# Kernel optimization log

Hardware: AMD Instinct MI355X
Metric: run time of the kernel (lower is better)

The kernel has to match this reference:

```python
import jax, jax.numpy as jnp
import numpy as np

DELTA_VAR = 0.5
DELTA_DIST = 1.5
ALPHA, BETA, GAMMA = 1.0, 1.0, 0.001
NUM_CLUSTERS = 16  # labels in [0, 16); all assumed present per sample (N >> C)

B, F, N = 32, 8, 131072


def _l1(x, axis):
    return jnp.sum(jnp.abs(x), axis=axis)  # norm=1 in the original module


def _discriminative_loss(x, target):
    # x: (B, F, N) float, target: (B, N) int labels in [0, C)
    b, f, n = x.shape
    c = NUM_CLUSTERS
    # flatten batch+cluster into one segment id space
    seg = (target + jnp.arange(b, dtype=target.dtype)[:, None] * c).reshape(-1)  # (B*N,)
    x_flat = x.transpose(0, 2, 1).reshape(b * n, f)  # (B*N, F)

    sums = jax.ops.segment_sum(x_flat, seg, num_segments=b * c)              # (B*C, F)
    counts = jax.ops.segment_sum(jnp.ones((b * n,), x.dtype), seg, num_segments=b * c)
    present = counts > 0
    safe_cnt = jnp.where(present, counts, 1.0)
    means_c = sums / safe_cnt[:, None]                                        # (B*C, F) per-cluster means

    # per-point cluster mean (== c_means tensor in torch, shape (B,F,N) there)
    means_pt = means_c[seg]                                                   # (B*N, F)

    # variance term: hinge(||x - mean||_1 - delta_var)^2, averaged per cluster, summed
    var = jnp.maximum(_l1(x_flat - means_pt, axis=1) - DELTA_VAR, 0.0) ** 2   # (B*N,)
    var_sums = jax.ops.segment_sum(var, seg, num_segments=b * c)
    # NOTE: torch version's division by num_clusters is a discarded no-op -> only /bs
    var_term = jnp.sum(jnp.where(present, var_sums / safe_cnt, 0.0)) / b

    # distance term: torch indexes c_means[i][:, unique_labels]; with labels 0..C-1
    # present, unique == arange(C), i.e. the per-point means at point indices 0..C-1
    mc = means_pt.reshape(b, n, f)[:, :c, :]                                  # (B, C, F)
    d = _l1(mc[:, :, None, :] - mc[:, None, :, :], axis=-1)                   # (B, C, C)
    margin = 2.0 * DELTA_DIST * (1.0 - jnp.eye(c, dtype=x.dtype))             # (C, C)
    dist = jnp.sum(jnp.maximum(margin[None] - d, 0.0) ** 2, axis=(1, 2)) / (c * (c - 1))
    dist_term = jnp.sum(dist) / b

    # regularization: mean over (distinct) cluster means of their L1 norm
    mcC = means_c.reshape(b, c, f)
    reg_term = jnp.sum(jnp.mean(_l1(mcC, axis=-1), axis=1)) / b

    return ALPHA * var_term + BETA * dist_term + GAMMA * reg_term


def setup_inputs() -> dict:
    key = jax.random.key(0)
    kx, kt = jax.random.split(key)
    x = jax.random.normal(kx, (B, F, N), dtype=jnp.float32)
    target = jax.random.randint(kt, (B, N), 0, NUM_CLUSTERS, dtype=jnp.int64)
    return {"input": x, "target": target}


def reference(input, target):
    return _discriminative_loss(input, target)
```

## Files before the change

kernel.cpp:

```cpp
#include <hip/hip_runtime.h>

#define BB 32
#define FF 8
#define NN 131072
#define CC 16

#define CHUNKS 64
#define POINTS (NN / CHUNKS)
#define NBLK   (CHUNKS * BB)

constexpr float DELTA_VAR  = 0.5f;
constexpr float DELTA_DIST = 1.5f;
constexpr float ALPHA = 1.0f, BETA = 1.0f, GAMMA = 0.001f;

#define PSLOT    160
#define WS_PART  0
#define WS_VARP  (NBLK * PSLOT)
#define WS_MEANS (WS_VARP + NBLK)

__global__ __launch_bounds__(256) void k_sums(const float* __restrict__ x,
                                              const int* __restrict__ tgt,
                                              float* __restrict__ ws) {
    __shared__ float priv[256 * 34];
    __shared__ float cpriv[64 * 17];
    const int tid = threadIdx.x;
#pragma unroll
    for (int i = 0; i < 34; ++i) priv[tid * 34 + i] = 0.f;
    if (tid < 64) {
#pragma unroll
        for (int i = 0; i < 16; ++i) cpriv[tid * 17 + i] = 0.f;
    }
    __syncthreads();

    const int b  = blockIdx.y;
    const int ch = blockIdx.x;
    const int fp = tid >> 6;
    const int g  = tid & 63;
    const int n0 = ch * POINTS;
    const float* __restrict__ xf0 = x + (size_t)b * FF * NN + (size_t)(2 * fp) * NN;
    const float* __restrict__ xf1 = xf0 + NN;
    const int*   __restrict__ tb  = tgt + (size_t)b * NN;
    const int base  = tid * 34;
    const int cbase = g * 17;

#pragma unroll 2
    for (int k = 0; k < POINTS / 128; ++k) {
        const int n = n0 + k * 128 + g * 2;
        const int2   t2 = *reinterpret_cast<const int2*>(tb + n);
        const float2 v0 = *reinterpret_cast<const float2*>(xf0 + n);
        const float2 v1 = *reinterpret_cast<const float2*>(xf1 + n);
        {
            float2* p = reinterpret_cast<float2*>(&priv[base + 2 * t2.x]);
            float2 cur = *p; cur.x += v0.x; cur.y += v1.x; *p = cur;
        }
        {
            float2* p = reinterpret_cast<float2*>(&priv[base + 2 * t2.y]);
            float2 cur = *p; cur.x += v0.y; cur.y += v1.y; *p = cur;
        }
        if (fp == 0) {
            cpriv[cbase + t2.x] += 1.f;
            cpriv[cbase + t2.y] += 1.f;
        }
    }
    __syncthreads();

    float* const part = &ws[WS_PART + (size_t)(b * CHUNKS + ch) * PSLOT];
    if (tid < 128) {
        const int f = tid >> 4, c = tid & 15;
        const int pair = f >> 1, comp = f & 1;
        float s = 0.f;
#pragma unroll
        for (int gg = 0; gg < 64; ++gg)
            s += priv[(pair * 64 + gg) * 34 + 2 * c + comp];
        part[tid] = s;
    } else if (tid < 144) {
        const int rc = tid - 128;
        float s = 0.f;
#pragma unroll
        for (int gg = 0; gg < 64; ++gg) s += cpriv[gg * 17 + rc];
        part[tid] = s;
    }
}

__global__ __launch_bounds__(256) void k_var(const float* __restrict__ x,
                                             const int* __restrict__ tgt,
                                             float* __restrict__ ws) {
    __shared__ float sred[144];
    __shared__ float smf[CC * 12];
    __shared__ float sinv[CC];
    __shared__ float wsum[4];

    const int tid = threadIdx.x;
    const int b   = blockIdx.y;
    const int ch  = blockIdx.x;

    if (tid < 144) {
        const float* p = &ws[WS_PART + (size_t)b * CHUNKS * PSLOT + tid];
        float s = 0.f;
#pragma unroll 8
        for (int c2 = 0; c2 < CHUNKS; ++c2) s += p[(size_t)c2 * PSLOT];
        sred[tid] = s;
    }
    __syncthreads();
    if (tid < CC) {
        const float cnt = sred[128 + tid];
        sinv[tid] = cnt > 0.f ? 1.f / cnt : 0.f;
    }
    __syncthreads();
    if (tid < 128) {
        const int f = tid >> 4, c = tid & 15;
        const float m = sred[tid] * sinv[c];
        smf[c * 12 + f] = m;
        if (ch == 0) ws[WS_MEANS + ((size_t)b * CC + c) * FF + f] = m;
    }
    __syncthreads();

    const float4* sm4 = reinterpret_cast<const float4*>(smf);
    const int n0 = ch * POINTS;
    const float* __restrict__ xb = x + (size_t)b * FF * NN;
    const int*   __restrict__ tb = tgt + (size_t)b * NN;

    float acc = 0.f;
#pragma unroll
    for (int it = 0; it < 2; ++it) {
        const int n = n0 + tid * 4 + it * 1024;
        const int4 t4 = *reinterpret_cast<const int4*>(tb + n);
        const float4 A0 = sm4[3 * t4.x], B0 = sm4[3 * t4.x + 1];
        const float4 A1 = sm4[3 * t4.y], B1 = sm4[3 * t4.y + 1];
        const float4 A2 = sm4[3 * t4.z], B2 = sm4[3 * t4.z + 1];
        const float4 A3 = sm4[3 * t4.w], B3 = sm4[3 * t4.w + 1];
        float s0, s1, s2, s3;
        {
            const float4 v = *reinterpret_cast<const float4*>(xb + 0 * NN + n);
            s0 = fabsf(v.x - A0.x); s1 = fabsf(v.y - A1.x);
            s2 = fabsf(v.z - A2.x); s3 = fabsf(v.w - A3.x);
        }
        {
            const float4 v = *reinterpret_cast<const float4*>(xb + 1 * NN + n);
            s0 += fabsf(v.x - A0.y); s1 += fabsf(v.y - A1.y);
            s2 += fabsf(v.z - A2.y); s3 += fabsf(v.w - A3.y);
        }
        {
            const float4 v = *reinterpret_cast<const float4*>(xb + 2 * NN + n);
            s0 += fabsf(v.x - A0.z); s1 += fabsf(v.y - A1.z);
            s2 += fabsf(v.z - A2.z); s3 += fabsf(v.w - A3.z);
        }
        {
            const float4 v = *reinterpret_cast<const float4*>(xb + 3 * NN + n);
            s0 += fabsf(v.x - A0.w); s1 += fabsf(v.y - A1.w);
            s2 += fabsf(v.z - A2.w); s3 += fabsf(v.w - A3.w);
        }
        {
            const float4 v = *reinterpret_cast<const float4*>(xb + 4 * NN + n);
            s0 += fabsf(v.x - B0.x); s1 += fabsf(v.y - B1.x);
            s2 += fabsf(v.z - B2.x); s3 += fabsf(v.w - B3.x);
        }
        {
            const float4 v = *reinterpret_cast<const float4*>(xb + 5 * NN + n);
            s0 += fabsf(v.x - B0.y); s1 += fabsf(v.y - B1.y);
            s2 += fabsf(v.z - B2.y); s3 += fabsf(v.w - B3.y);
        }
        {
            const float4 v = *reinterpret_cast<const float4*>(xb + 6 * NN + n);
            s0 += fabsf(v.x - B0.z); s1 += fabsf(v.y - B1.z);
            s2 += fabsf(v.z - B2.z); s3 += fabsf(v.w - B3.z);
        }
        {
            const float4 v = *reinterpret_cast<const float4*>(xb + 7 * NN + n);
            s0 += fabsf(v.x - B0.w); s1 += fabsf(v.y - B1.w);
            s2 += fabsf(v.z - B2.w); s3 += fabsf(v.w - B3.w);
        }
        float h;
        h = fmaxf(s0 - DELTA_VAR, 0.f); acc += h * h * sinv[t4.x];
        h = fmaxf(s1 - DELTA_VAR, 0.f); acc += h * h * sinv[t4.y];
        h = fmaxf(s2 - DELTA_VAR, 0.f); acc += h * h * sinv[t4.z];
        h = fmaxf(s3 - DELTA_VAR, 0.f); acc += h * h * sinv[t4.w];
    }

#pragma unroll
    for (int off = 32; off > 0; off >>= 1) acc += __shfl_down(acc, off, 64);
    if ((tid & 63) == 0) wsum[tid >> 6] = acc;
    __syncthreads();
    if (tid == 0) ws[WS_VARP + b * CHUNKS + ch] = wsum[0] + wsum[1] + wsum[2] + wsum[3];
}

__global__ __launch_bounds__(512) void k_final(const int* __restrict__ tgt,
                                               const float* __restrict__ ws,
                                               float* __restrict__ out) {
    __shared__ float smeans[BB * CC * FF];
    __shared__ int   st[BB * CC];
    __shared__ float red[512];

    const int tid = threadIdx.x;
    const int b = tid >> 4;
    const int c = tid & 15;

    float l1 = 0.f;
#pragma unroll
    for (int f = 0; f < FF; ++f) {
        const float m = ws[WS_MEANS + ((size_t)b * CC + c) * FF + f];
        smeans[(b * CC + c) * FF + f] = m;
        l1 += fabsf(m);
    }
    st[b * CC + c] = tgt[(size_t)b * NN + c];

    float varp = 0.f;
#pragma unroll
    for (int i = 0; i < NBLK / 512; ++i) varp += ws[WS_VARP + i * 512 + tid];

    float contrib = (GAMMA / (float)(CC * BB)) * l1 + (ALPHA / (float)BB) * varp;
    __syncthreads();

    const int ti = st[b * CC + c];
    float mi[FF];
#pragma unroll
    for (int f = 0; f < FF; ++f) mi[f] = smeans[(b * CC + ti) * FF + f];

    float dsum = 0.f;
    for (int j = 0; j < CC; ++j) {
        const int tj = st[b * CC + j];
        float d = 0.f;
#pragma unroll
        for (int f = 0; f < FF; ++f) d += fabsf(mi[f] - smeans[(b * CC + tj) * FF + f]);
        if (j != c) {
            const float h = 2.f * DELTA_DIST - d;
            if (h > 0.f) dsum += h * h;
        }
    }
    contrib += (BETA / (float)(CC * (CC - 1) * BB)) * dsum;

    red[tid] = contrib;
    __syncthreads();
    for (int s = 256; s > 0; s >>= 1) {
        if (tid < s) red[tid] += red[tid + s];
        __syncthreads();
    }
    if (tid == 0) out[0] = red[0];
}

extern "C" void kernel_launch(void* const* d_in, const int* in_sizes, int n_in,
                              void* d_out, int out_size, void* d_ws, size_t ws_size,
                              hipStream_t stream) {
    const float* x  = (const float*)d_in[0];
    const int* tgt  = (const int*)d_in[1];
    float* out = (float*)d_out;
    float* ws  = (float*)d_ws;

    dim3 grid(CHUNKS, BB);
    k_sums<<<grid, 256, 0, stream>>>(x, tgt, ws);
    k_var <<<grid, 256, 0, stream>>>(x, tgt, ws);
    k_final<<<1, 512, 0, stream>>>(tgt, ws, out);
}
```

Before: 61.65 us.

## Fold final reduction kernel into variance kernel via atomics and last-block detection

Removes the separate single-block final kernel. The distance and regularization terms are now computed by the chunk-0 block of each batch inside the variance kernel. Per-batch partials are accumulated with atomics, and the last block to finish, found through an atomic counter, writes the output. This drops one launch and its serial tail, at the cost of atomic traffic and the counters being zeroed in the first kernel.

```diff
diff --git a/kernel.cpp b/kernel.cpp
--- a/kernel.cpp
+++ b/kernel.cpp
@@ -15,15 +15,24 @@
 
 #define PSLOT    160
 #define WS_PART  0
-#define WS_VARP  (NBLK * PSLOT)
-#define WS_MEANS (WS_VARP + NBLK)
+#define NPART    (NBLK * PSLOT)
+#define WS_VARB  NPART
+#define WS_DRG   (NPART + 32)
+#define WS_CNTI  (NPART + 64)
 
 __global__ __launch_bounds__(256) void k_sums(const float* __restrict__ x,
                                               const int* __restrict__ tgt,
-                                              float* __restrict__ ws) {
+                                              float* __restrict__ ws,
+                                              int* __restrict__ wsi) {
     __shared__ float priv[256 * 34];
     __shared__ float cpriv[64 * 17];
     const int tid = threadIdx.x;
+    const int b  = blockIdx.y;
+    const int ch = blockIdx.x;
+
+    if (ch == 0 && tid == 0) { ws[WS_VARB + b] = 0.f; ws[WS_DRG + b] = 0.f; }
+    if (ch == 0 && b == 0 && tid == 1) wsi[WS_CNTI] = 0;
+
 #pragma unroll
     for (int i = 0; i < 34; ++i) priv[tid * 34 + i] = 0.f;
     if (tid < 64) {
@@ -32,8 +41,6 @@
     }
     __syncthreads();
 
-    const int b  = blockIdx.y;
-    const int ch = blockIdx.x;
     const int fp = tid >> 6;
     const int g  = tid & 63;
     const int n0 = ch * POINTS;
@@ -84,11 +91,16 @@
 
 __global__ __launch_bounds__(256) void k_var(const float* __restrict__ x,
                                              const int* __restrict__ tgt,
-                                             float* __restrict__ ws) {
+                                             float* __restrict__ ws,
+                                             int* __restrict__ wsi,
+                                             float* __restrict__ out) {
     __shared__ float sred[144];
     __shared__ float smf[CC * 12];
     __shared__ float sinv[CC];
     __shared__ float wsum[4];
+    __shared__ float sdist[CC];
+    __shared__ int   sst[CC];
+    __shared__ int   lastflag;
 
     const int tid = threadIdx.x;
     const int b   = blockIdx.y;
@@ -101,6 +113,7 @@
         for (int c2 = 0; c2 < CHUNKS; ++c2) s += p[(size_t)c2 * PSLOT];
         sred[tid] = s;
     }
+    if (ch == 0 && tid >= 144 && tid < 160) sst[tid - 144] = tgt[(size_t)b * NN + (tid - 144)];
     __syncthreads();
     if (tid < CC) {
         const float cnt = sred[128 + tid];
@@ -109,11 +122,33 @@
     __syncthreads();
     if (tid < 128) {
         const int f = tid >> 4, c = tid & 15;
-        const float m = sred[tid] * sinv[c];
-        smf[c * 12 + f] = m;
-        if (ch == 0) ws[WS_MEANS + ((size_t)b * CC + c) * FF + f] = m;
-    }
-    __syncthreads();
+        smf[c * 12 + f] = sred[tid] * sinv[c];
+    }
+    __syncthreads();
+
+    if (ch == 0 && tid < CC) {
+        const int c = tid;
+        float l1 = 0.f;
+#pragma unroll
+        for (int f = 0; f < FF; ++f) l1 += fabsf(smf[c * 12 + f]);
+        const int ti = sst[c];
+        float mi[FF];
+#pragma unroll
+        for (int f = 0; f < FF; ++f) mi[f] = smf[ti * 12 + f];
+        float dsum = 0.f;
+        for (int j = 0; j < CC; ++j) {
+            const int tj = sst[j];
+            float d = 0.f;
+#pragma unroll
+            for (int f = 0; f < FF; ++f) d += fabsf(mi[f] - smf[tj * 12 + f]);
+            if (j != c) {
+                const float h = 2.f * DELTA_DIST - d;
+                if (h > 0.f) dsum += h * h;
+            }
+        }
+        sdist[c] = (GAMMA / (float)(CC * BB)) * l1
+                 + (BETA / (float)(CC * (CC - 1) * BB)) * dsum;
+    }
 
     const float4* sm4 = reinterpret_cast<const float4*>(smf);
     const int n0 = ch * POINTS;
@@ -181,61 +216,30 @@
     for (int off = 32; off > 0; off >>= 1) acc += __shfl_down(acc, off, 64);
     if ((tid & 63) == 0) wsum[tid >> 6] = acc;
     __syncthreads();
-    if (tid == 0) ws[WS_VARP + b * CHUNKS + ch] = wsum[0] + wsum[1] + wsum[2] + wsum[3];
-}
-
-__global__ __launch_bounds__(512) void k_final(const int* __restrict__ tgt,
-                                               const float* __restrict__ ws,
-                                               float* __restrict__ out) {
-    __shared__ float smeans[BB * CC * FF];
-    __shared__ int   st[BB * CC];
-    __shared__ float red[512];
-
-    const int tid = threadIdx.x;
-    const int b = tid >> 4;
-    const int c = tid & 15;
-
-    float l1 = 0.f;
-#pragma unroll
-    for (int f = 0; f < FF; ++f) {
-        const float m = ws[WS_MEANS + ((size_t)b * CC + c) * FF + f];
-        smeans[(b * CC + c) * FF + f] = m;
-        l1 += fabsf(m);
-    }
-    st[b * CC + c] = tgt[(size_t)b * NN + c];
-
-    float varp = 0.f;
-#pragma unroll
-    for (int i = 0; i < NBLK / 512; ++i) varp += ws[WS_VARP + i * 512 + tid];
-
-    float contrib = (GAMMA / (float)(CC * BB)) * l1 + (ALPHA / (float)BB) * varp;
-    __syncthreads();
-
-    const int ti = st[b * CC + c];
-    float mi[FF];
-#pragma unroll
-    for (int f = 0; f < FF; ++f) mi[f] = smeans[(b * CC + ti) * FF + f];
-
-    float dsum = 0.f;
-    for (int j = 0; j < CC; ++j) {
-        const int tj = st[b * CC + j];
-        float d = 0.f;
-#pragma unroll
-        for (int f = 0; f < FF; ++f) d += fabsf(mi[f] - smeans[(b * CC + tj) * FF + f]);
-        if (j != c) {
-            const float h = 2.f * DELTA_DIST - d;
-            if (h > 0.f) dsum += h * h;
-        }
-    }
-    contrib += (BETA / (float)(CC * (CC - 1) * BB)) * dsum;
-
-    red[tid] = contrib;
-    __syncthreads();
-    for (int s = 256; s > 0; s >>= 1) {
-        if (tid < s) red[tid] += red[tid + s];
-        __syncthreads();
-    }
-    if (tid == 0) out[0] = red[0];
+
+    if (tid == 0) {
+        atomicAdd(&ws[WS_VARB + b], wsum[0] + wsum[1] + wsum[2] + wsum[3]);
+        if (ch == 0) {
+            float drg = 0.f;
+#pragma unroll
+            for (int i = 0; i < CC; ++i) drg += sdist[i];
+            atomicAdd(&ws[WS_DRG + b], drg);
+        }
+        asm volatile("s_waitcnt vmcnt(0)" ::: "memory");
+        lastflag = (atomicAdd(&wsi[WS_CNTI], 1) == NBLK - 1);
+    }
+    __syncthreads();
+    if (lastflag && tid < 64) {
+        float val = 0.f;
+        if (tid < BB) {
+            const float v = atomicAdd(&ws[WS_VARB + tid], 0.f);
+            const float d = atomicAdd(&ws[WS_DRG + tid], 0.f);
+            val = (ALPHA / (float)BB) * v + d;
+        }
+#pragma unroll
+        for (int off = 16; off > 0; off >>= 1) val += __shfl_down(val, off, 64);
+        if (tid == 0) out[0] = val;
+    }
 }
 
 extern "C" void kernel_launch(void* const* d_in, const int* in_sizes, int n_in,
@@ -245,9 +249,9 @@
     const int* tgt  = (const int*)d_in[1];
     float* out = (float*)d_out;
     float* ws  = (float*)d_ws;
+    int*   wsi = (int*)d_ws;
 
     dim3 grid(CHUNKS, BB);
-    k_sums<<<grid, 256, 0, stream>>>(x, tgt, ws);
-    k_var <<<grid, 256, 0, stream>>>(x, tgt, ws);
-    k_final<<<1, 512, 0, stream>>>(tgt, ws, out);
+    k_sums<<<grid, 256, 0, stream>>>(x, tgt, ws, wsi);
+    k_var <<<grid, 256, 0, stream>>>(x, tgt, ws, wsi, out);
 }
```

New measurement: 68.94 us. 11.8% more time.
